# Kernel optimization log

Measured on AMD Instinct MI355X. Metric: run time of the kernel, lower is better.

Reference implementation:

```python
import jax, jax.numpy as jnp
import numpy as np

L, B, T, C, H, V = 6, 8, 1024, 1024, 16, 4096
HS = C // H  # head size = 64


def _ln(x, g, b):
    mu = x.mean(-1, keepdims=True)
    var = ((x - mu) ** 2).mean(-1, keepdims=True)
    return (x - mu) * jax.lax.rsqrt(var + 1e-5) * g + b


def setup_inputs() -> dict:
    key = jax.random.key(0)
    ks = jax.random.split(key, 12)
    s = 0.02
    return {
        "idx": jax.random.randint(ks[0], (B, T), 0, V),
        "tok_emb": jax.random.normal(ks[1], (V, C), jnp.float32) * s,
        "pos_emb": jax.random.normal(ks[2], (T, C), jnp.float32) * s,
        "Wq": jax.random.normal(ks[3], (L, C, C), jnp.float32) * s,
        "Wk": jax.random.normal(ks[4], (L, C, C), jnp.float32) * s,
        "Wv": jax.random.normal(ks[5], (L, C, C), jnp.float32) * s,
        "Wo": jax.random.normal(ks[6], (L, C, C), jnp.float32) * s,
        "bo": jnp.zeros((L, C), jnp.float32),
        "ln1_g": jnp.ones((L, C), jnp.float32),
        "ln1_b": jnp.zeros((L, C), jnp.float32),
        "ln2_g": jnp.ones((L, C), jnp.float32),
        "ln2_b": jnp.zeros((L, C), jnp.float32),
        "W1": jax.random.normal(ks[7], (L, C, 4 * C), jnp.float32) * s,
        "b1": jnp.zeros((L, 4 * C), jnp.float32),
        "W2": jax.random.normal(ks[8], (L, 4 * C, C), jnp.float32) * s,
        "b2": jnp.zeros((L, C), jnp.float32),
        "lnf_g": jnp.ones((C,), jnp.float32),
        "lnf_b": jnp.zeros((C,), jnp.float32),
        "lm_w": jax.random.normal(ks[9], (C, V), jnp.float32) * s,
        "lm_b": jnp.zeros((V,), jnp.float32),
    }


def _gpt(idx, tok_emb, pos_emb, Wq, Wk, Wv, Wo, bo, ln1_g, ln1_b, ln2_g, ln2_b,
         W1, b1, W2, b2, lnf_g, lnf_b, lm_w, lm_b):
    x = tok_emb[idx] + pos_emb[None, :idx.shape[1]]  # (B,T,C)
    mask = jnp.tril(jnp.ones((T, T), bool))
    neg_inf = jnp.float32(-jnp.inf)

    def block(x, p):
        wq, wk, wv, wo, bo_, g1, be1, g2, be2, w1, bb1, w2, bb2 = p
        h = _ln(x, g1, be1)
        # per-head projections (no bias), heads concatenated along feature dim
        q = (h @ wq).reshape(B, T, H, HS)
        k = (h @ wk).reshape(B, T, H, HS)
        v = (h @ wv).reshape(B, T, H, HS)
        # NOTE: faithful to source -- scores are MULTIPLIED by sqrt(head_size)
        att = jnp.einsum('bqhd,bkhd->bhqk', q, k) * (HS ** 0.5)
        att = jnp.where(mask, att, neg_inf)
        p_att = jax.nn.softmax(att, axis=-1)  # dropout is identity at eval
        o = jnp.einsum('bhqk,bkhd->bqhd', p_att, v).reshape(B, T, C)
        x = x + o @ wo + bo_
        h2 = _ln(x, g2, be2)
        x = x + jax.nn.relu(h2 @ w1 + bb1) @ w2 + bb2
        return x, None

    x, _ = jax.lax.scan(
        block, x,
        (Wq, Wk, Wv, Wo, bo, ln1_g, ln1_b, ln2_g, ln2_b, W1, b1, W2, b2))
    x = _ln(x, lnf_g, lnf_b)
    return x @ lm_w + lm_b  # logits (B,T,V)


def reference(idx, tok_emb, pos_emb, Wq, Wk, Wv, Wo, bo, ln1_g, ln1_b, ln2_g,
              ln2_b, W1, b1, W2, b2, lnf_g, lnf_b, lm_w, lm_b):
    return _gpt(idx, tok_emb, pos_emb, Wq, Wk, Wv, Wo, bo, ln1_g, ln1_b,
                ln2_g, ln2_b, W1, b1, W2, b2, lnf_g, lnf_b, lm_w, lm_b)
```

## Files before the change

kernel.cpp:

```cpp
#include <hip/hip_runtime.h>

#define LL 6
#define BB 8
#define TT 1024
#define CC 1024
#define HH 16
#define HS 64
#define VV 4096
#define BT (BB*TT)

typedef __attribute__((ext_vector_type(4))) float f32x4;
typedef __attribute__((ext_vector_type(8))) short bf16x8;

__device__ __forceinline__ float bf2f(unsigned short u) {
  union { unsigned int u; float f; } v; v.u = ((unsigned int)u) << 16; return v.f;
}
__device__ __forceinline__ unsigned short rne16(float f) {
  unsigned u = __float_as_uint(f);
  return (unsigned short)((u + 0x7fffu + ((u >> 16) & 1u)) >> 16);
}
__device__ __forceinline__ void gld16(const uint4* g, uint4* l) {
  __builtin_amdgcn_global_load_lds(
      (const __attribute__((address_space(1))) void*)g,
      (__attribute__((address_space(3))) void*)l, 16, 0, 0);
}

__global__ __launch_bounds__(256) void embed_kernel(
    const int* __restrict__ idx, const float* __restrict__ tok,
    const float* __restrict__ pos, float* __restrict__ x) {
  int bt = blockIdx.x;
  int t = bt & (TT - 1);
  int id = idx[bt];
  float4 te = reinterpret_cast<const float4*>(tok)[(size_t)id * (CC/4) + threadIdx.x];
  float4 pe = reinterpret_cast<const float4*>(pos)[(size_t)t * (CC/4) + threadIdx.x];
  float4 r; r.x = te.x+pe.x; r.y = te.y+pe.y; r.z = te.z+pe.z; r.w = te.w+pe.w;
  reinterpret_cast<float4*>(x)[(size_t)bt * (CC/4) + threadIdx.x] = r;
}

struct Oct3 { uint4 p0, p1, p2; };
__device__ __forceinline__ unsigned pk2(unsigned lo, unsigned hi) {
  return (lo >> 16) | (hi & 0xffff0000u);
}
__device__ __forceinline__ Oct3 split8(const float* f) {
  unsigned a0[8], a1[8], a2[8];
  #pragma unroll
  for (int e = 0; e < 8; ++e) {
    float v = f[e];
    unsigned u = __float_as_uint(v);
    a0[e] = u;
    float r = v - __uint_as_float(u & 0xffff0000u);
    unsigned ur = __float_as_uint(r);
    a1[e] = ur;
    float r2 = r - __uint_as_float(ur & 0xffff0000u);
    a2[e] = __float_as_uint(r2);
  }
  Oct3 o;
  o.p0 = make_uint4(pk2(a0[0],a0[1]), pk2(a0[2],a0[3]), pk2(a0[4],a0[5]), pk2(a0[6],a0[7]));
  o.p1 = make_uint4(pk2(a1[0],a1[1]), pk2(a1[2],a1[3]), pk2(a1[4],a1[5]), pk2(a1[6],a1[7]));
  o.p2 = make_uint4(pk2(a2[0],a2[1]), pk2(a2[2],a2[3]), pk2(a2[4],a2[5]), pk2(a2[6],a2[7]));
  return o;
}
struct Oct2 { uint4 p0, p1; };
__device__ __forceinline__ Oct2 split8_rne2(const float* f) {
  unsigned h0[8], h1[8];
  #pragma unroll
  for (int e = 0; e < 8; ++e) {
    h0[e] = rne16(f[e]);
    float r = f[e] - bf2f((unsigned short)h0[e]);
    h1[e] = rne16(r);
  }
  Oct2 o;
  o.p0 = make_uint4(h0[0]|(h0[1]<<16), h0[2]|(h0[3]<<16), h0[4]|(h0[5]<<16), h0[6]|(h0[7]<<16));
  o.p1 = make_uint4(h1[0]|(h1[1]<<16), h1[2]|(h1[3]<<16), h1[4]|(h1[5]<<16), h1[6]|(h1[7]<<16));
  return o;
}
__device__ __forceinline__ uint4 pack8_rne(const float* f) {
  unsigned h[8];
  #pragma unroll
  for (int e = 0; e < 8; ++e) h[e] = rne16(f[e]);
  return make_uint4(h[0]|(h[1]<<16), h[2]|(h[3]<<16), h[4]|(h[5]<<16), h[6]|(h[7]<<16));
}

__global__ __launch_bounds__(256) void ln32_kernel(
    const float* __restrict__ x, const float* __restrict__ g,
    const float* __restrict__ b, float* __restrict__ out) {
  __shared__ float red[8];
  int row = blockIdx.x, tid = threadIdx.x;
  float4 v = reinterpret_cast<const float4*>(x)[(size_t)row * (CC/4) + tid];
  float s  = v.x+v.y+v.z+v.w;
  float ss = v.x*v.x+v.y*v.y+v.z*v.z+v.w*v.w;
  #pragma unroll
  for (int off = 32; off; off >>= 1) { s += __shfl_xor(s, off); ss += __shfl_xor(ss, off); }
  if ((tid & 63) == 0) { red[tid>>6] = s; red[4+(tid>>6)] = ss; }
  __syncthreads();
  s  = red[0]+red[1]+red[2]+red[3];
  ss = red[4]+red[5]+red[6]+red[7];
  float mu = s * (1.f/CC);
  float rs = rsqrtf(ss*(1.f/CC) - mu*mu + 1e-5f);
  float4 gg = reinterpret_cast<const float4*>(g)[tid];
  float4 bb = reinterpret_cast<const float4*>(b)[tid];
  float4 o;
  o.x = (v.x-mu)*rs*gg.x + bb.x;
  o.y = (v.y-mu)*rs*gg.y + bb.y;
  o.z = (v.z-mu)*rs*gg.z + bb.z;
  o.w = (v.w-mu)*rs*gg.w + bb.w;
  reinterpret_cast<float4*>(out)[(size_t)row * (CC/4) + tid] = o;
}

__global__ __launch_bounds__(256) void lnsplit_kernel(
    const float* __restrict__ x, const float* __restrict__ g,
    const float* __restrict__ b, uint4* __restrict__ outp) {
  __shared__ float red[8];
  __shared__ float rowbuf[1024];
  int row = blockIdx.x, tid = threadIdx.x;
  float4 v = reinterpret_cast<const float4*>(x)[(size_t)row * (CC/4) + tid];
  float s  = v.x+v.y+v.z+v.w;
  float ss = v.x*v.x+v.y*v.y+v.z*v.z+v.w*v.w;
  #pragma unroll
  for (int off = 32; off; off >>= 1) { s += __shfl_xor(s, off); ss += __shfl_xor(ss, off); }
  if ((tid & 63) == 0) { red[tid>>6] = s; red[4+(tid>>6)] = ss; }
  __syncthreads();
  s  = red[0]+red[1]+red[2]+red[3];
  ss = red[4]+red[5]+red[6]+red[7];
  float mu = s * (1.f/CC);
  float rs = rsqrtf(ss*(1.f/CC) - mu*mu + 1e-5f);
  float4 gg = reinterpret_cast<const float4*>(g)[tid];
  float4 bb = reinterpret_cast<const float4*>(b)[tid];
  float4 o;
  o.x = (v.x-mu)*rs*gg.x + bb.x;
  o.y = (v.y-mu)*rs*gg.y + bb.y;
  o.z = (v.z-mu)*rs*gg.z + bb.z;
  o.w = (v.w-mu)*rs*gg.w + bb.w;
  *reinterpret_cast<float4*>(&rowbuf[tid*4]) = o;
  __syncthreads();
  if (tid < 128) {
    const size_t aPS = (size_t)128 * 16 * 512;
    int kt = tid >> 3, sl = tid & 7;
    int r = row & 63, mt = row >> 6;
    float f[8];
    #pragma unroll
    for (int e = 0; e < 8; ++e) f[e] = rowbuf[tid*8 + e];
    size_t di = ((size_t)(mt*16 + kt))*512 + r*8 + (sl ^ (r & 7));
    Oct2 ot = split8_rne2(f);
    outp[di] = ot.p0; outp[aPS+di] = ot.p1;
  }
}

template<int NP>
__global__ __launch_bounds__(256) void bsplit_kernel(
    const float* __restrict__ Bw, uint4* __restrict__ outp, int ldb,
    int ntile0, int ntTotal) {
  int ntile = ntile0 + blockIdx.x, kt = blockIdx.y;
  size_t planeStride = (size_t)ntTotal * gridDim.y * 1024;
  int tid = threadIdx.x;
  int bcol = tid & 127, bkcg = tid >> 7;
  #pragma unroll
  for (int g = 0; g < 4; ++g) {
    int kc = bkcg*4 + g;
    float f[8];
    #pragma unroll
    for (int j = 0; j < 8; ++j)
      f[j] = Bw[(size_t)(kt*64 + kc*8 + j) * ldb + blockIdx.x*128 + bcol];
    size_t di = (((size_t)ntile * gridDim.y + kt) * 8 + kc) * 128 + bcol;
    if (NP == 2) {
      Oct2 o = split8_rne2(f);
      outp[di] = o.p0; outp[planeStride+di] = o.p1;
    } else {
      outp[di] = pack8_rne(f);
    }
  }
}

template<int NP, bool ASP, int NM>
__global__ __launch_bounds__(256) void gemm128_kernel(
    const float* __restrict__ A, int lda,
    const uint4* __restrict__ Asp, size_t aPS,
    const uint4* __restrict__ Bs,
    const float* __restrict__ bias, const float* __restrict__ res,
    float* __restrict__ outf, int K, int ldc, int relu,
    int ntile0, int ntTotal, int kt0, int ktTotal, int vtmode,
    uint4* __restrict__ kout) {
  __shared__ uint4 lds_all[NP*2048];
  uint4* lds_a = lds_all;
  uint4* lds_b = lds_all + NP*1024;
  int tid = threadIdx.x;
  int by = blockIdx.y;
  int m0 = by * 128;
  int n0 = blockIdx.x * 128;
  int ntg = ntile0 + blockIdx.x;
  size_t bPS = (size_t)ntTotal * ktTotal * 1024;
  int lane = tid & 63, w = tid >> 6;
  int wm = w >> 1, wn = w & 1;
  int lr = lane & 15, lk = lane >> 4;
  int nkt = K >> 6;

  f32x4 acc[4][4];
  #pragma unroll
  for (int m = 0; m < 4; ++m)
    #pragma unroll
    for (int n = 0; n < 4; ++n)
      acc[m][n] = (f32x4){0.f, 0.f, 0.f, 0.f};

  for (int kt = 0; kt < nkt; ++kt) {
    if (ASP) {
      #pragma unroll
      for (int p = 0; p < NP; ++p) {
        const uint4* s0 = Asp + p*aPS + ((size_t)(2*by)   * nkt + kt)*512;
        const uint4* s1 = Asp + p*aPS + ((size_t)(2*by+1) * nkt + kt)*512;
        #pragma unroll
        for (int i = 0; i < 2; ++i) {
          int ch = w*2 + i;
          gld16(s0 + ch*64 + lane, &lds_a[p*1024 + ch*64]);
          gld16(s1 + ch*64 + lane, &lds_a[p*1024 + 512 + ch*64]);
        }
      }
    } else {
      #pragma unroll
      for (int i = 0; i < 4; ++i) {
        int c = tid + i * 256;
        int row = c >> 3, sl = c & 7;
        const float4* ap = reinterpret_cast<const float4*>(
            A + (size_t)(m0+row)*lda + kt*64 + sl*8);
        float4 x0 = ap[0], x1 = ap[1];
        float f[8] = {x0.x,x0.y,x0.z,x0.w,x1.x,x1.y,x1.z,x1.w};
        int di = (row>>6)*512 + (row&63)*8 + (sl ^ (row & 7));
        if (NP == 2) {
          Oct2 o = split8_rne2(f);
          lds_a[di] = o.p0; lds_a[1024 + di] = o.p1;
        } else {
          lds_a[di] = pack8_rne(f);
        }
      }
    }
    {
      int ktg = kt0 + kt;
      #pragma unroll
      for (int p = 0; p < NP; ++p) {
        const uint4* sb = Bs + p*bPS + ((size_t)ntg * ktTotal + ktg)*1024;
        #pragma unroll
        for (int i = 0; i < 4; ++i) {
          int ch = w*4 + i;
          gld16(sb + ch*64 + lane, &lds_b[p*1024 + ch*64]);
        }
      }
    }
    __syncthreads();
    #pragma unroll
    for (int ks = 0; ks < 2; ++ks) {
      int kc = ks*4 + lk;
      bf16x8 af[NP][4], bfr[NP][4];
      #pragma unroll
      for (int m = 0; m < 4; ++m) {
        int row = wm*64 + m*16 + lr;
        int si = (row>>6)*512 + (row&63)*8 + (kc ^ (row & 7));
        #pragma unroll
        for (int p = 0; p < NP; ++p)
          af[p][m] = reinterpret_cast<const bf16x8*>(lds_a + p*1024)[si];
      }
      #pragma unroll
      for (int n = 0; n < 4; ++n) {
        int si = kc*128 + wn*64 + n*16 + lr;
        #pragma unroll
        for (int p = 0; p < NP; ++p)
          bfr[p][n] = reinterpret_cast<const bf16x8*>(lds_b + p*1024)[si];
      }
      #pragma unroll
      for (int m = 0; m < 4; ++m)
        #pragma unroll
        for (int n = 0; n < 4; ++n) {
          acc[m][n] = __builtin_amdgcn_mfma_f32_16x16x32_bf16(af[0][m], bfr[0][n], acc[m][n], 0, 0, 0);
          if (NP == 2) {
            acc[m][n] = __builtin_amdgcn_mfma_f32_16x16x32_bf16(af[0][m], bfr[1][n], acc[m][n], 0, 0, 0);
            acc[m][n] = __builtin_amdgcn_mfma_f32_16x16x32_bf16(af[1][m], bfr[0][n], acc[m][n], 0, 0, 0);
            if (NM == 4)
              acc[m][n] = __builtin_amdgcn_mfma_f32_16x16x32_bf16(af[1][m], bfr[1][n], acc[m][n], 0, 0, 0);
          }
        }
    }
    __syncthreads();
  }

  if (vtmode == 1) {
    char* vb = (char*)outf;
    const size_t VPSb = (size_t)2048 * 512 * 16;
    #pragma unroll
    for (int m = 0; m < 4; ++m) {
      int row = m0 + wm*64 + m*16 + lk*4;
      int bq = row >> 10;
      int t  = row & (TT-1);
      int ktile = t >> 6, r = t & 63;
      int kc = r >> 3, toct0 = r & 7;
      #pragma unroll
      for (int n = 0; n < 4; ++n) {
        int col = n0 + wn*64 + n*16 + lr;
        int hh2 = col >> 6, d = col & 63;
        int tile = (bq*HH + hh2)*16 + ktile;
        int vi = kc*64 + ((d ^ (kc<<1)) & 63);
        unsigned p0[4], p1[4];
        #pragma unroll
        for (int j = 0; j < 4; ++j) {
          float v = acc[m][n][j];
          p0[j] = rne16(v);
          p1[j] = rne16(v - bf2f((unsigned short)p0[j]));
        }
        uint2 w0 = make_uint2(p0[0]|(p0[1]<<16), p0[2]|(p0[3]<<16));
        uint2 w1 = make_uint2(p1[0]|(p1[1]<<16), p1[2]|(p1[3]<<16));
        char* base = vb + ((size_t)tile*512 + vi)*16 + toct0*2;
        *reinterpret_cast<uint2*>(base) = w0;
        *reinterpret_cast<uint2*>(base + VPSb) = w1;
      }
    }
  } else if (vtmode == 2) {
    float* bounce = (float*)lds_all;
    #pragma unroll
    for (int m = 0; m < 4; ++m)
      #pragma unroll
      for (int n = 0; n < 4; ++n) {
        int cl = wn*64 + n*16 + lr;
        float bv = bias[n0 + cl];
        #pragma unroll
        for (int j = 0; j < 4; ++j) {
          int rl = wm*64 + m*16 + lk*4 + j;
          bounce[rl*128 + cl] = fmaxf(acc[m][n][j] + bv, 0.f);
        }
      }
    __syncthreads();
    uint4* a1p = (uint4*)outf;
    const size_t aPSa = (size_t)128 * 32 * 512;
    #pragma unroll
    for (int i = 0; i < 8; ++i) {
      int ot = tid + i*256;
      int r = ot >> 4, o = ot & 15;
      float f[8];
      #pragma unroll
      for (int e = 0; e < 8; ++e) f[e] = bounce[r*128 + o*8 + e];
      Oct2 o2 = split8_rne2(f);
      int mt = 2*by + (r>>6), rs = r & 63;
      int ktg = (n0 >> 6) + (o >> 3), sl = o & 7;
      size_t di = ((size_t)(mt*32 + ktg))*512 + rs*8 + (sl ^ (rs & 7));
      a1p[di] = o2.p0; a1p[aPSa + di] = o2.p1;
    }
  } else if (vtmode == 3 && ntg >= 8) {
    float* bounce = (float*)lds_all;
    #pragma unroll
    for (int m = 0; m < 4; ++m)
      #pragma unroll
      for (int n = 0; n < 4; ++n) {
        int cl = wn*64 + n*16 + lr;
        #pragma unroll
        for (int j = 0; j < 4; ++j) {
          int rl = wm*64 + m*16 + lk*4 + j;
          bounce[rl*128 + cl] = acc[m][n][j];
        }
      }
    __syncthreads();
    const size_t KPSC = (size_t)2048 * 512;
    int bq = m0 >> 10;
    int kt0tok = (m0 & 1023) >> 6;
    int hh0 = (ntg - 8) * 2;
    #pragma unroll
    for (int i = 0; i < 8; ++i) {
      int u = tid + i*256;
      int r = u >> 4, oct = u & 15;
      int head = oct >> 3, sl = oct & 7;
      float f[8];
      #pragma unroll
      for (int e = 0; e < 8; ++e) f[e] = bounce[r*128 + head*64 + sl*8 + e];
      Oct2 o = split8_rne2(f);
      int rk = r & 63;
      int tile = (bq*HH + hh0 + head)*16 + kt0tok + (r >> 6);
      size_t di = (size_t)tile*512 + rk*8 + (sl ^ (rk & 7));
      kout[di] = o.p0; kout[KPSC + di] = o.p1;
    }
  } else {
    #pragma unroll
    for (int m = 0; m < 4; ++m) {
      #pragma unroll
      for (int n = 0; n < 4; ++n) {
        int col = n0 + wn*64 + n*16 + lr;
        float bv = bias ? bias[col] : 0.f;
        #pragma unroll
        for (int j = 0; j < 4; ++j) {
          int row = m0 + wm*64 + m*16 + lk*4 + j;
          float vv = acc[m][n][j] + bv;
          if (relu) vv = fmaxf(vv, 0.f);
          size_t off = (size_t)row * ldc + col;
          if (res) vv += res[off];
          outf[off] = vv;
        }
      }
    }
  }
}

__global__ __launch_bounds__(256) void attn_mfma_kernel(
    const float* __restrict__ qf, const uint4* __restrict__ Kp,
    const uint4* __restrict__ Vp, uint4* __restrict__ aout) {
  __shared__ uint4 K_lds[2][512];
  __shared__ uint4 V_lds[2][512];
  __shared__ unsigned P_lds[64*68];
  const size_t KPS = (size_t)2048 * 512;
  const size_t VPS = (size_t)2048 * 512;
  const size_t APS = (size_t)128 * 16 * 512;
  int tid = threadIdx.x, lane = tid & 63, w = tid >> 6;
  int rid = blockIdx.x;
  int qt = 15 - (rid & 15), hh = (rid >> 4) & 15, b = rid >> 8;
  int lr = lane & 15, lk = lane >> 4;
  const size_t tok0 = (size_t)b * TT;

  bf16x8 qa[2][3];
  {
    const float* qp = qf + (tok0 + qt*64 + w*16 + lr) * 1024 + hh*HS;
    #pragma unroll
    for (int ks = 0; ks < 2; ++ks) {
      const float4* p4 = reinterpret_cast<const float4*>(qp + ks*32 + lk*8);
      float4 a = p4[0], c = p4[1];
      float f[8] = {a.x,a.y,a.z,a.w,c.x,c.y,c.z,c.w};
      Oct3 ot = split8(f);
      qa[ks][0] = *reinterpret_cast<bf16x8*>(&ot.p0);
      qa[ks][1] = *reinterpret_cast<bf16x8*>(&ot.p1);
      qa[ks][2] = *reinterpret_cast<bf16x8*>(&ot.p2);
    }
  }

  float mrow[4] = {-3.0e38f,-3.0e38f,-3.0e38f,-3.0e38f};
  float lrow[4] = {0.f,0.f,0.f,0.f};
  f32x4 oac[4];
  #pragma unroll
  for (int n = 0; n < 4; ++n) oac[n] = (f32x4){0.f,0.f,0.f,0.f};

  for (int kt = 0; kt <= qt; ++kt) {
    __syncthreads();
    {
      int tile = ((b*HH + hh)*16 + kt);
      const uint4* ksrc = Kp + (size_t)tile*512;
      #pragma unroll
      for (int p = 0; p < 2; ++p)
        #pragma unroll
        for (int i = 0; i < 2; ++i) {
          int ch = w*2 + i;
          gld16(ksrc + p*KPS + ch*64 + lane, &K_lds[p][ch*64]);
        }
      const uint4* vsrc = Vp + (size_t)tile*512;
      #pragma unroll
      for (int p = 0; p < 2; ++p)
        #pragma unroll
        for (int i = 0; i < 2; ++i) {
          int ch = w*2 + i;
          gld16(vsrc + p*VPS + ch*64 + lane, &V_lds[p][ch*64]);
        }
    }
    __syncthreads();

    f32x4 sfr[4];
    #pragma unroll
    for (int nf = 0; nf < 4; ++nf) sfr[nf] = (f32x4){0.f,0.f,0.f,0.f};
    #pragma unroll
    for (int ks = 0; ks < 2; ++ks) {
      int kc = ks*4 + lk;
      #pragma unroll
      for (int nf = 0; nf < 4; ++nf) {
        int row = nf*16 + lr;
        int si = row*8 + (kc ^ (row & 7));
        bf16x8 k0 = *reinterpret_cast<const bf16x8*>(&K_lds[0][si]);
        bf16x8 k1 = *reinterpret_cast<const bf16x8*>(&K_lds[1][si]);
        sfr[nf] = __builtin_amdgcn_mfma_f32_16x16x32_bf16(qa[ks][0], k0, sfr[nf], 0,0,0);
        sfr[nf] = __builtin_amdgcn_mfma_f32_16x16x32_bf16(qa[ks][0], k1, sfr[nf], 0,0,0);
        sfr[nf] = __builtin_amdgcn_mfma_f32_16x16x32_bf16(qa[ks][1], k0, sfr[nf], 0,0,0);
        sfr[nf] = __builtin_amdgcn_mfma_f32_16x16x32_bf16(qa[ks][1], k1, sfr[nf], 0,0,0);
        sfr[nf] = __builtin_amdgcn_mfma_f32_16x16x32_bf16(qa[ks][2], k0, sfr[nf], 0,0,0);
      }
    }
    #pragma unroll
    for (int nf = 0; nf < 4; ++nf)
      #pragma unroll
      for (int j = 0; j < 4; ++j) {
        float s = sfr[nf][j] * 8.0f;
        if (kt == qt && (nf*16 + lr) > (w*16 + lk*4 + j)) s = -3.0e38f;
        sfr[nf][j] = s;
      }
    float alpha[4], tsum[4];
    #pragma unroll
    for (int j = 0; j < 4; ++j) {
      float mx = fmaxf(fmaxf(sfr[0][j], sfr[1][j]), fmaxf(sfr[2][j], sfr[3][j]));
      mx = fmaxf(mx, __shfl_xor(mx, 1));
      mx = fmaxf(mx, __shfl_xor(mx, 2));
      mx = fmaxf(mx, __shfl_xor(mx, 4));
      mx = fmaxf(mx, __shfl_xor(mx, 8));
      float mnew = fmaxf(mrow[j], mx);
      alpha[j] = __expf(mrow[j] - mnew);
      mrow[j] = mnew;
      tsum[j] = 0.f;
    }
    #pragma unroll
    for (int nf = 0; nf < 4; ++nf)
      #pragma unroll
      for (int j = 0; j < 4; ++j) {
        float p = __expf(sfr[nf][j] - mrow[j]);
        tsum[j] += p;
        unsigned u = __float_as_uint(p);
        float r = p - __uint_as_float(u & 0xffff0000u);
        unsigned pw = (u & 0xffff0000u) | (__float_as_uint(r) >> 16);
        int qrow = w*16 + lk*4 + j;
        int kcol = nf*16 + lr;
        P_lds[qrow*68 + (((kcol>>3) ^ (qrow & 7)))*8 + (kcol & 7)] = pw;
      }
    #pragma unroll
    for (int j = 0; j < 4; ++j) {
      float ts = tsum[j];
      ts += __shfl_xor(ts, 1);
      ts += __shfl_xor(ts, 2);
      ts += __shfl_xor(ts, 4);
      ts += __shfl_xor(ts, 8);
      lrow[j] = lrow[j]*alpha[j] + ts;
      oac[0][j] *= alpha[j]; oac[1][j] *= alpha[j];
      oac[2][j] *= alpha[j]; oac[3][j] *= alpha[j];
    }
    __syncthreads();

    #pragma unroll
    for (int ks = 0; ks < 2; ++ks) {
      int kc = ks*4 + lk;
      int prow = w*16 + lr;
      const uint4* pp4 = reinterpret_cast<const uint4*>(
          &P_lds[prow*68 + ((kc ^ (prow & 7)))*8]);
      uint4 pw0 = pp4[0], pw1 = pp4[1];
      uint4 phu, plu;
      phu.x = (pw0.x>>16) | (pw0.y & 0xffff0000u);
      phu.y = (pw0.z>>16) | (pw0.w & 0xffff0000u);
      phu.z = (pw1.x>>16) | (pw1.y & 0xffff0000u);
      phu.w = (pw1.z>>16) | (pw1.w & 0xffff0000u);
      plu.x = (pw0.x & 0xffffu) | (pw0.y << 16);
      plu.y = (pw0.z & 0xffffu) | (pw0.w << 16);
      plu.z = (pw1.x & 0xffffu) | (pw1.y << 16);
      plu.w = (pw1.z & 0xffffu) | (pw1.w << 16);
      bf16x8 ph = *reinterpret_cast<bf16x8*>(&phu);
      bf16x8 pl = *reinterpret_cast<bf16x8*>(&plu);
      #pragma unroll
      for (int nf2 = 0; nf2 < 4; ++nf2) {
        int d = nf2*16 + lr;
        int vi = kc*64 + ((d ^ (kc<<1)) & 63);
        bf16x8 vh = *reinterpret_cast<const bf16x8*>(&V_lds[0][vi]);
        bf16x8 vl = *reinterpret_cast<const bf16x8*>(&V_lds[1][vi]);
        oac[nf2] = __builtin_amdgcn_mfma_f32_16x16x32_bf16(ph, vh, oac[nf2], 0,0,0);
        oac[nf2] = __builtin_amdgcn_mfma_f32_16x16x32_bf16(ph, vl, oac[nf2], 0,0,0);
        oac[nf2] = __builtin_amdgcn_mfma_f32_16x16x32_bf16(pl, vh, oac[nf2], 0,0,0);
      }
    }
  }

  __syncthreads();
  float* Pf = (float*)P_lds;
  #pragma unroll
  for (int j = 0; j < 4; ++j) {
    float inv = 1.0f / lrow[j];
    #pragma unroll
    for (int nf2 = 0; nf2 < 4; ++nf2)
      Pf[(w*16 + lk*4 + j)*68 + nf2*16 + lr] = oac[nf2][j] * inv;
  }
  __syncthreads();
  int mtkt = (b*16 + qt)*16 + hh;
  #pragma unroll
  for (int i = 0; i < 2; ++i) {
    int u = tid + i*256;
    int r = u >> 3, sl = u & 7;
    float f[8];
    #pragma unroll
    for (int e = 0; e < 8; ++e) f[e] = Pf[r*68 + sl*8 + e];
    Oct2 o = split8_rne2(f);
    size_t di = (size_t)mtkt*512 + r*8 + (sl ^ (r & 7));
    aout[di] = o.p0; aout[APS + di] = o.p1;
  }
}

extern "C" void kernel_launch(void* const* d_in, const int* in_sizes, int n_in,
                              void* d_out, int out_size, void* d_ws, size_t ws_size,
                              hipStream_t stream) {
  const int*   idx  = (const int*)d_in[0];
  const float* tok  = (const float*)d_in[1];
  const float* pos  = (const float*)d_in[2];
  const float* Wq   = (const float*)d_in[3];
  const float* Wk   = (const float*)d_in[4];
  const float* Wv   = (const float*)d_in[5];
  const float* Wo   = (const float*)d_in[6];
  const float* bo   = (const float*)d_in[7];
  const float* ln1g = (const float*)d_in[8];
  const float* ln1b = (const float*)d_in[9];
  const float* ln2g = (const float*)d_in[10];
  const float* ln2b = (const float*)d_in[11];
  const float* W1   = (const float*)d_in[12];
  const float* b1   = (const float*)d_in[13];
  const float* W2   = (const float*)d_in[14];
  const float* b2   = (const float*)d_in[15];
  const float* lnfg = (const float*)d_in[16];
  const float* lnfb = (const float*)d_in[17];
  const float* lmw  = (const float*)d_in[18];
  const float* lmb  = (const float*)d_in[19];
  float* out = (float*)d_out;

  char* ob = (char*)d_out;
  float* x  = (float*)ob;
  float* vplanes = (float*)(ob + ((size_t)32<<20));
  float* qf = (float*)(ob + ((size_t)64<<20));
  uint4* Kp = (uint4*)(ob + ((size_t)96<<20));
  float* a1p = (float*)(ob + ((size_t)64<<20));
  char* wsb = (char*)d_ws;
  uint4* aspH  = (uint4*)wsb;
  uint4* bsQK  = (uint4*)(wsb + ((size_t)32<<20));
  uint4* bsV   = (uint4*)(wsb + ((size_t)40<<20));
  uint4* bsO   = (uint4*)(wsb + ((size_t)44<<20));
  uint4* aspH2 = (uint4*)wsb;
  uint4* aspH3 = (uint4*)wsb;
  uint4* bsW1  = (uint4*)(wsb + ((size_t)32<<20));
  uint4* bsW2  = (uint4*)(wsb + ((size_t)48<<20));
  float* hf    = (float*)wsb;
  uint4* bsL   = (uint4*)(wsb + ((size_t)32<<20));
  const size_t aPSh = (size_t)128 * 16 * 512;
  const size_t aPSa = (size_t)128 * 32 * 512;

  dim3 blk(256);
  dim3 gQK(16, 64), gV(8, 64), gO(8, 64);
  dim3 gW1(16, 64), gW2(8, 64), gL(32, 64);
  dim3 s8(8, 16), sW1(32, 16), sW2(8, 64), sLM(32, 16);

  embed_kernel<<<BT, blk, 0, stream>>>(idx, tok, pos, x);
  for (int l = 0; l < LL; ++l) {
    const float* Wq_l = Wq + (size_t)l*CC*CC;
    const float* Wk_l = Wk + (size_t)l*CC*CC;
    const float* Wv_l = Wv + (size_t)l*CC*CC;
    const float* Wo_l = Wo + (size_t)l*CC*CC;
    const float* W1_l = W1 + (size_t)l*CC*4*CC;
    const float* W2_l = W2 + (size_t)l*4*CC*CC;
    lnsplit_kernel<<<BT, blk, 0, stream>>>(x, ln1g + (size_t)l*CC, ln1b + (size_t)l*CC, aspH);
    bsplit_kernel<2><<<s8, blk, 0, stream>>>(Wq_l, bsQK, CC, 0, 16);
    bsplit_kernel<2><<<s8, blk, 0, stream>>>(Wk_l, bsQK, CC, 8, 16);
    bsplit_kernel<2><<<s8, blk, 0, stream>>>(Wv_l, bsV, CC, 0, 8);
    bsplit_kernel<2><<<s8, blk, 0, stream>>>(Wo_l, bsO, CC, 0, 8);
    gemm128_kernel<2,true,4><<<gQK, blk, 0, stream>>>(nullptr, 0, aspH, aPSh, bsQK,
        nullptr, nullptr, qf, CC, 1024, 0, 0, 16, 0, 16, 3, Kp);
    gemm128_kernel<2,true,3><<<gV, blk, 0, stream>>>(nullptr, 0, aspH, aPSh, bsV,
        nullptr, nullptr, vplanes, CC, CC, 0, 0, 8, 0, 16, 1, nullptr);
    attn_mfma_kernel<<<BB*HH*16, blk, 0, stream>>>(qf, Kp, (const uint4*)vplanes, aspH2);
    gemm128_kernel<2,true,3><<<gO, blk, 0, stream>>>(nullptr, 0, aspH2, aPSh, bsO,
        bo + (size_t)l*CC, x, x, CC, CC, 0, 0, 8, 0, 16, 0, nullptr);
    lnsplit_kernel<<<BT, blk, 0, stream>>>(x, ln2g + (size_t)l*CC, ln2b + (size_t)l*CC, aspH3);
    bsplit_kernel<2><<<sW1, blk, 0, stream>>>(W1_l, bsW1, 4*CC, 0, 32);
    bsplit_kernel<2><<<sW2, blk, 0, stream>>>(W2_l, bsW2, CC, 0, 8);
    gemm128_kernel<2,true,3><<<gW1, blk, 0, stream>>>(nullptr, 0, aspH3, aPSh, bsW1,
        b1 + (size_t)l*4*CC, nullptr, a1p, CC, 2048, 1, 0, 32, 0, 16, 2, nullptr);
    gemm128_kernel<2,true,3><<<gW2, blk, 0, stream>>>(nullptr, 0, (const uint4*)a1p, aPSa, bsW2,
        b2 + (size_t)l*CC, x, x, 2048, CC, 0, 0, 8, 0, 64, 0, nullptr);
    gemm128_kernel<2,true,3><<<gW1, blk, 0, stream>>>(nullptr, 0, aspH3, aPSh, bsW1,
        b1 + (size_t)l*4*CC + 2048, nullptr, a1p, CC, 2048, 1, 16, 32, 0, 16, 2, nullptr);
    gemm128_kernel<2,true,3><<<gW2, blk, 0, stream>>>(nullptr, 0, (const uint4*)a1p, aPSa, bsW2,
        nullptr, x, x, 2048, CC, 0, 0, 8, 32, 64, 0, nullptr);
  }
  ln32_kernel<<<BT, blk, 0, stream>>>(x, lnfg, lnfb, hf);
  bsplit_kernel<1><<<sLM, blk, 0, stream>>>(lmw, bsL, VV, 0, 32);
  gemm128_kernel<1,false,1><<<gL, blk, 0, stream>>>(hf, CC, nullptr, 0, bsL,
      lmb, nullptr, out, CC, VV, 0, 0, 32, 0, 16, 0, nullptr);
}
```

Baseline: 5.099 ms.

## Cut QK split-bf16 passes, merge weight-split launches, remap attention blocks to XCDs

The QK^T score computation drops from a three-term to a two-term split-bf16 scheme: Q is split into two RNE planes and only three cross products are kept instead of five, which cuts MFMA work per tile. The four per-layer weight-split launches are merged into one launch that uses a z-indexed grid, reducing launch overhead. Attention block indices are remapped so each XCD receives whole (batch, head) groups, which should improve L2 reuse of K/V tiles. The reduced-precision score path could increase numerical error, and the error is amplified by the sqrt(head_size) multiplier on the scores.

```diff
diff --git a/kernel.cpp b/kernel.cpp
--- a/kernel.cpp
+++ b/kernel.cpp
@@ -143,6 +143,32 @@
     size_t di = ((size_t)(mt*16 + kt))*512 + r*8 + (sl ^ (r & 7));
     Oct2 ot = split8_rne2(f);
     outp[di] = ot.p0; outp[aPS+di] = ot.p1;
+  }
+}
+
+__global__ __launch_bounds__(256) void bsplit4_kernel(
+    const float* __restrict__ Wq, const float* __restrict__ Wk,
+    const float* __restrict__ Wv, const float* __restrict__ Wo,
+    uint4* __restrict__ bsQK, uint4* __restrict__ bsV, uint4* __restrict__ bsO) {
+  int z = blockIdx.z;
+  const float* Bw = (z == 0) ? Wq : (z == 1) ? Wk : (z == 2) ? Wv : Wo;
+  uint4* outp = (z <= 1) ? bsQK : (z == 2) ? bsV : bsO;
+  int ntile0 = (z == 1) ? 8 : 0;
+  int ntTotal = (z <= 1) ? 16 : 8;
+  int ntile = ntile0 + blockIdx.x, kt = blockIdx.y;
+  size_t planeStride = (size_t)ntTotal * 16 * 1024;
+  int tid = threadIdx.x;
+  int bcol = tid & 127, bkcg = tid >> 7;
+  #pragma unroll
+  for (int g = 0; g < 4; ++g) {
+    int kc = bkcg*4 + g;
+    float f[8];
+    #pragma unroll
+    for (int j = 0; j < 8; ++j)
+      f[j] = Bw[(size_t)(kt*64 + kc*8 + j) * CC + blockIdx.x*128 + bcol];
+    size_t di = (((size_t)ntile * 16 + kt) * 8 + kc) * 128 + bcol;
+    Oct2 o = split8_rne2(f);
+    outp[di] = o.p0; outp[planeStride+di] = o.p1;
   }
 }
 
@@ -403,12 +429,14 @@
   const size_t VPS = (size_t)2048 * 512;
   const size_t APS = (size_t)128 * 16 * 512;
   int tid = threadIdx.x, lane = tid & 63, w = tid >> 6;
-  int rid = blockIdx.x;
-  int qt = 15 - (rid & 15), hh = (rid >> 4) & 15, b = rid >> 8;
+  int i = blockIdx.x;
+  int xcd = i & 7, qm = (i >> 3) & 15, ghi = i >> 7;
+  int g = ghi*8 + xcd;
+  int b = g >> 4, hh = g & 15, qt = 15 - qm;
   int lr = lane & 15, lk = lane >> 4;
   const size_t tok0 = (size_t)b * TT;
 
-  bf16x8 qa[2][3];
+  bf16x8 qa[2][2];
   {
     const float* qp = qf + (tok0 + qt*64 + w*16 + lr) * 1024 + hh*HS;
     #pragma unroll
@@ -416,10 +444,9 @@
       const float4* p4 = reinterpret_cast<const float4*>(qp + ks*32 + lk*8);
       float4 a = p4[0], c = p4[1];
       float f[8] = {a.x,a.y,a.z,a.w,c.x,c.y,c.z,c.w};
-      Oct3 ot = split8(f);
+      Oct2 ot = split8_rne2(f);
       qa[ks][0] = *reinterpret_cast<bf16x8*>(&ot.p0);
       qa[ks][1] = *reinterpret_cast<bf16x8*>(&ot.p1);
-      qa[ks][2] = *reinterpret_cast<bf16x8*>(&ot.p2);
     }
   }
 
@@ -437,16 +464,16 @@
       #pragma unroll
       for (int p = 0; p < 2; ++p)
         #pragma unroll
-        for (int i = 0; i < 2; ++i) {
-          int ch = w*2 + i;
+        for (int i2 = 0; i2 < 2; ++i2) {
+          int ch = w*2 + i2;
           gld16(ksrc + p*KPS + ch*64 + lane, &K_lds[p][ch*64]);
         }
       const uint4* vsrc = Vp + (size_t)tile*512;
       #pragma unroll
       for (int p = 0; p < 2; ++p)
         #pragma unroll
-        for (int i = 0; i < 2; ++i) {
-          int ch = w*2 + i;
+        for (int i2 = 0; i2 < 2; ++i2) {
+          int ch = w*2 + i2;
           gld16(vsrc + p*VPS + ch*64 + lane, &V_lds[p][ch*64]);
         }
     }
@@ -467,8 +494,6 @@
         sfr[nf] = __builtin_amdgcn_mfma_f32_16x16x32_bf16(qa[ks][0], k0, sfr[nf], 0,0,0);
         sfr[nf] = __builtin_amdgcn_mfma_f32_16x16x32_bf16(qa[ks][0], k1, sfr[nf], 0,0,0);
         sfr[nf] = __builtin_amdgcn_mfma_f32_16x16x32_bf16(qa[ks][1], k0, sfr[nf], 0,0,0);
-        sfr[nf] = __builtin_amdgcn_mfma_f32_16x16x32_bf16(qa[ks][1], k1, sfr[nf], 0,0,0);
-        sfr[nf] = __builtin_amdgcn_mfma_f32_16x16x32_bf16(qa[ks][2], k0, sfr[nf], 0,0,0);
       }
     }
     #pragma unroll
@@ -561,8 +586,8 @@
   __syncthreads();
   int mtkt = (b*16 + qt)*16 + hh;
   #pragma unroll
-  for (int i = 0; i < 2; ++i) {
-    int u = tid + i*256;
+  for (int i2 = 0; i2 < 2; ++i2) {
+    int u = tid + i2*256;
     int r = u >> 3, sl = u & 7;
     float f[8];
     #pragma unroll
@@ -621,7 +646,7 @@
   dim3 blk(256);
   dim3 gQK(16, 64), gV(8, 64), gO(8, 64);
   dim3 gW1(16, 64), gW2(8, 64), gL(32, 64);
-  dim3 s8(8, 16), sW1(32, 16), sW2(8, 64), sLM(32, 16);
+  dim3 s4(8, 16, 4), sW1(32, 16), sW2(8, 64), sLM(32, 16);
 
   embed_kernel<<<BT, blk, 0, stream>>>(idx, tok, pos, x);
   for (int l = 0; l < LL; ++l) {
@@ -632,10 +657,7 @@
     const float* W1_l = W1 + (size_t)l*CC*4*CC;
     const float* W2_l = W2 + (size_t)l*4*CC*CC;
     lnsplit_kernel<<<BT, blk, 0, stream>>>(x, ln1g + (size_t)l*CC, ln1b + (size_t)l*CC, aspH);
-    bsplit_kernel<2><<<s8, blk, 0, stream>>>(Wq_l, bsQK, CC, 0, 16);
-    bsplit_kernel<2><<<s8, blk, 0, stream>>>(Wk_l, bsQK, CC, 8, 16);
-    bsplit_kernel<2><<<s8, blk, 0, stream>>>(Wv_l, bsV, CC, 0, 8);
-    bsplit_kernel<2><<<s8, blk, 0, stream>>>(Wo_l, bsO, CC, 0, 8);
+    bsplit4_kernel<<<s4, blk, 0, stream>>>(Wq_l, Wk_l, Wv_l, Wo_l, bsQK, bsV, bsO);
     gemm128_kernel<2,true,4><<<gQK, blk, 0, stream>>>(nullptr, 0, aspH, aPSh, bsQK,
         nullptr, nullptr, qf, CC, 1024, 0, 0, 16, 0, 16, 3, Kp);
     gemm128_kernel<2,true,3><<<gV, blk, 0, stream>>>(nullptr, 0, aspH, aPSh, bsV,
```

Measured after the change: 4.720 ms. 7.4% less time.
